# Kernel optimization log

Hardware: AMD Instinct MI355X
Metric: run time of the kernel (lower is better)

Reference implementation:

```python
import jax, jax.numpy as jnp
import numpy as np

PENALTY_LAMBDA = 0.5
MAX_RULES = 512
INIT_GATE_LOGIT = -2.0


def setup_inputs() -> dict:
    key = jax.random.key(0)
    k1, k2, k3 = jax.random.split(key, 3)
    B, V, E = 64, 128000, 1000000
    logits = jax.random.normal(k1, (B, V), dtype=jnp.float32)
    # learned per-rule gate logits (nn.Parameter initialized at init_gate_logit;
    # we perturb slightly so gradients are non-degenerate)
    gate_logits = jnp.full((MAX_RULES,), INIT_GATE_LOGIT, dtype=jnp.float32) \
        + 0.1 * jax.random.normal(k2, (MAX_RULES,), dtype=jnp.float32)
    # flattened ragged (rule, token) violation pairs
    kr, kt = jax.random.split(k3)
    rule_ids = jax.random.randint(kr, (E,), 0, MAX_RULES, dtype=jnp.int32)
    token_ids = jax.random.randint(kt, (E,), 0, V, dtype=jnp.int32)
    return {"logits": logits, "gate_logits": gate_logits,
            "rule_ids": rule_ids, "token_ids": token_ids}


def reference(logits, gate_logits, rule_ids, token_ids):
    # eval-mode binary concrete gate (no noise, no thresholding): sigmoid(logit)
    gates = jax.nn.sigmoid(gate_logits)                      # [R]
    V = logits.shape[-1]
    # gated penalty value per (rule, token) pair, single vectorized scatter-add
    vals = gates[rule_ids] * jnp.asarray(PENALTY_LAMBDA, logits.dtype)  # [E]
    pen_1d = jnp.zeros((V,), dtype=logits.dtype).at[token_ids].add(vals)  # [V]
    penalties = jnp.broadcast_to(pen_1d[None, :], logits.shape)           # [B,V]
    modified = logits - penalties
    # coverage loss: -mean of gates over rules that fire (have >=1 violation)
    firing = jnp.zeros((MAX_RULES,), dtype=logits.dtype).at[rule_ids].set(1.0)
    n_firing = jnp.maximum(firing.sum(), 1.0)
    coverage_loss = -(gates * firing).sum() / n_firing
    return modified, coverage_loss, penalties
```

## Files before the change

### kernel.cpp

```cpp
#include <hip/hip_runtime.h>

#define PENALTY_LAMBDA 0.5f
#define RULES 512
#define NR 4
#define RS 32000
#define VOCAB 128000
#define G 64
#define NQ 2

typedef float f32x4 __attribute__((ext_vector_type(4)));


__global__ void __launch_bounds__(512) scatter_kernel(
    const int* __restrict__ rule_ids, const int* __restrict__ token_ids,
    const float* __restrict__ gate_logits, float* __restrict__ partials,
    unsigned* __restrict__ masks, int E) {
    __shared__ __align__(16) float hist[RS];
    __shared__ float s_g[RULES];
    __shared__ unsigned char s_f[RULES];
    int t = threadIdx.x;
    int g = blockIdx.x;
    int r = blockIdx.y;
    for (int i = t; i < RS; i += 512) hist[i] = 0.f;
    if (t < RULES) {
        float x = gate_logits[t];
        s_g[t] = PENALTY_LAMBDA / (1.0f + expf(-x));
    }
    if (t < RULES / 4) ((unsigned*)s_f)[t] = 0u;
    __syncthreads();

    const int lo = r * RS;
    const int stride = G * 512 * 4;
    for (int base = (g * 512 + t) * 4; base + 4 <= E; base += stride) {
        int4 tt = *(const int4*)(token_ids + base);
        int4 rr = *(const int4*)(rule_ids + base);
        int ts[4] = {tt.x, tt.y, tt.z, tt.w};
        int rv[4] = {rr.x, rr.y, rr.z, rr.w};
#pragma unroll
        for (int k = 0; k < 4; ++k) {
            int tok = ts[k] - lo;
            if ((unsigned)tok < (unsigned)RS) atomicAdd(&hist[tok], s_g[rv[k]]);
            if (r == 0) s_f[rv[k]] = 1;
        }
    }
    if (g == 0 && t == 0) {
        for (int e = E & ~3; e < E; ++e) {
            int tok = token_ids[e] - lo; int ru = rule_ids[e];
            if ((unsigned)tok < (unsigned)RS) atomicAdd(&hist[tok], s_g[ru]);
            if (r == 0) s_f[ru] = 1;
        }
    }
    __syncthreads();

    float* dst = partials + ((size_t)r * G + g) * RS;
    for (int i = t * 4; i < RS; i += 512 * 4)
        *(f32x4*)(dst + i) = *(const f32x4*)(&hist[i]);

    if (r == 0 && t < 16) {
        const unsigned* w = (const unsigned*)s_f + t * 8;
        unsigned m = 0;
#pragma unroll
        for (int k = 0; k < 8; ++k) {
            unsigned d = w[k];
            if (d & 0x000000FFu) m |= 1u << (k * 4 + 0);
            if (d & 0x0000FF00u) m |= 1u << (k * 4 + 1);
            if (d & 0x00FF0000u) m |= 1u << (k * 4 + 2);
            if (d & 0xFF000000u) m |= 1u << (k * 4 + 3);
        }
        masks[g * 16 + t] = m;
    }
}

__global__ void __launch_bounds__(256) reduce_loss_kernel(
    const float* __restrict__ partials, const unsigned* __restrict__ masks,
    const float* __restrict__ gate_logits,
    float* __restrict__ penh, float* __restrict__ out_loss) {
    int t = threadIdx.x;
    int q = blockIdx.y;
    int j = blockIdx.x * 256 + t;
    int v0 = j << 2;
    int r = v0 / RS, bin = v0 - r * RS;
    const float* basep = partials + ((size_t)r * G + (size_t)q * (G / NQ)) * RS + bin;
    f32x4 s = {0.f, 0.f, 0.f, 0.f};
#pragma unroll 4
    for (int g = 0; g < G / NQ; ++g)
        s += *(const f32x4*)(basep + (size_t)g * RS);
    *(f32x4*)(penh + (size_t)q * VOCAB + v0) = s;

    if (blockIdx.x == 0 && q == 0) {
        __shared__ unsigned s_mask[16];
        __shared__ float sg[4], sf[4];
        if (t < 16) {
            unsigned m = 0;
            for (int g = 0; g < G; ++g) m |= masks[g * 16 + t];
            s_mask[t] = m;
        }
        __syncthreads();
        float f = 0.f, gf = 0.f;
        for (int i = t; i < RULES; i += 256) {
            float fb = ((s_mask[i >> 5] >> (i & 31)) & 1u) ? 1.f : 0.f;
            f += fb;
            gf += fb / (1.f + expf(-gate_logits[i]));
        }
        for (int off = 32; off > 0; off >>= 1) {
            gf += __shfl_down(gf, off, 64);
            f  += __shfl_down(f,  off, 64);
        }
        if ((t & 63) == 0) { sg[t >> 6] = gf; sf[t >> 6] = f; }
        __syncthreads();
        if (t == 0) {
            float tg = sg[0] + sg[1] + sg[2] + sg[3];
            float tf = sf[0] + sf[1] + sf[2] + sf[3];
            *out_loss = -tg / fmaxf(tf, 1.0f);
        }
    }
}

__global__ void __launch_bounds__(256) broadcast_kernel(
    const float* __restrict__ logits, const float* __restrict__ penh,
    float* __restrict__ out_mod, float* __restrict__ out_pen) {
    int j = blockIdx.x * 256 + threadIdx.x;
    int b = blockIdx.y;
    int v0 = j << 2;
    size_t base = (size_t)b * VOCAB + v0;
    f32x4 p0 = *(const f32x4*)(penh + v0) + *(const f32x4*)(penh + VOCAB + v0);
    f32x4 l = *(const f32x4*)(logits + base);
    *(f32x4*)(out_mod + base) = l - p0;

    bool lastj = (j == VOCAB / 4 - 1);
    f32x4 p1;
    if (lastj)
        p1 = *(const f32x4*)(penh) + *(const f32x4*)(penh + VOCAB);
    else
        p1 = *(const f32x4*)(penh + v0 + 4) + *(const f32x4*)(penh + VOCAB + v0 + 4);
    f32x4 ps = {p0.w, p1.x, p1.y, p1.z};
    if (lastj && b == (int)gridDim.y - 1) {
        out_pen[base + 3] = p0.w;
    } else {
        *(f32x4*)(out_pen + base + 3) = ps;
    }
    if (j == 0 && b == 0) {
        out_pen[0] = p0.x; out_pen[1] = p0.y; out_pen[2] = p0.z;
    }
}

extern "C" void kernel_launch(void* const* d_in, const int* in_sizes, int n_in,
                              void* d_out, int out_size, void* d_ws, size_t ws_size,
                              hipStream_t stream) {
    const float* logits      = (const float*)d_in[0];
    const float* gate_logits = (const float*)d_in[1];
    const int*   rule_ids    = (const int*)d_in[2];
    const int*   token_ids   = (const int*)d_in[3];
    float* out = (float*)d_out;

    const int E = in_sizes[2];
    const int V = VOCAB;
    const int B = in_sizes[0] / V;
    const size_t BV = (size_t)B * (size_t)V;

    float*    partials = (float*)d_ws;
    float*    penh     = partials + (size_t)NR * G * RS;
    unsigned* masks    = (unsigned*)(penh + (size_t)NQ * VOCAB);

    scatter_kernel<<<dim3(G, NR), 512, 0, stream>>>(
        rule_ids, token_ids, gate_logits, partials, masks, E);

    reduce_loss_kernel<<<dim3(V / 4 / 256, NQ), 256, 0, stream>>>(
        partials, masks, gate_logits, penh, out + BV);

    broadcast_kernel<<<dim3(V / 4 / 256, B), 256, 0, stream>>>(
        logits, penh, out, out + BV + 1);
}
```

Baseline: 130.4 us.

## Fuse partial-histogram reduction, loss, and broadcast into one kernel

New measurement: 122.4 us. 6.1% less time.

```diff
diff --git a/kernel.cpp b/kernel.cpp
--- a/kernel.cpp
+++ b/kernel.cpp
@@ -6,7 +6,9 @@
 #define RS 32000
 #define VOCAB 128000
 #define G 64
-#define NQ 2
+#define NB 64
+#define CH 500
+#define CJ 125
 
 typedef float f32x4 __attribute__((ext_vector_type(4)));
 
@@ -71,37 +73,61 @@
     }
 }
 
-__global__ void __launch_bounds__(256) reduce_loss_kernel(
+__global__ void __launch_bounds__(512) fused_kernel(
     const float* __restrict__ partials, const unsigned* __restrict__ masks,
-    const float* __restrict__ gate_logits,
-    float* __restrict__ penh, float* __restrict__ out_loss) {
+    const float* __restrict__ gate_logits, const float* __restrict__ logits,
+    float* __restrict__ out_mod, float* __restrict__ out_pen,
+    float* __restrict__ out_loss) {
+    __shared__ float s_pc[CH + 4];
+    __shared__ f32x4 s_part[4][CJ + 1];
     int t = threadIdx.x;
-    int q = blockIdx.y;
-    int j = blockIdx.x * 256 + t;
-    int v0 = j << 2;
-    int r = v0 / RS, bin = v0 - r * RS;
-    const float* basep = partials + ((size_t)r * G + (size_t)q * (G / NQ)) * RS + bin;
-    f32x4 s = {0.f, 0.f, 0.f, 0.f};
+    int tx = t & 127, ty = t >> 7;
+    int chunk = blockIdx.x;
+    int c0 = chunk * CH;
+    int r = c0 / RS;
+    int bin = c0 - r * RS;
+
+    {
+        f32x4 acc = {0.f, 0.f, 0.f, 0.f};
+        if (tx < CJ) {
+            const float* bp = partials + (size_t)r * G * RS + bin + tx * 4
+                            + (size_t)(ty * 16) * RS;
 #pragma unroll 4
-    for (int g = 0; g < G / NQ; ++g)
-        s += *(const f32x4*)(basep + (size_t)g * RS);
-    *(f32x4*)(penh + (size_t)q * VOCAB + v0) = s;
+            for (int g = 0; g < 16; ++g)
+                acc += *(const f32x4*)(bp + (size_t)g * RS);
+            s_part[ty][tx] = acc;
+        } else if (tx == 127) {
+            f32x4 e = {0.f, 0.f, 0.f, 0.f};
+            for (int i = 0; i < 4; ++i) {
+                int gb = c0 + CH + i; if (gb >= VOCAB) gb -= VOCAB;
+                int r2 = gb / RS, b2 = gb - r2 * RS;
+                const float* bp2 = partials + (size_t)r2 * G * RS + b2
+                                 + (size_t)(ty * 16) * RS;
+                float s = 0.f;
+                for (int g = 0; g < 16; ++g) s += bp2[(size_t)g * RS];
+                ((float*)&e)[i] = s;
+            }
+            s_part[ty][CJ] = e;
+        }
+    }
+    __syncthreads();
+    if (t < CJ + 1) {
+        f32x4 s = s_part[0][t] + s_part[1][t] + s_part[2][t] + s_part[3][t];
+        *(f32x4*)(s_pc + t * 4) = s;
+    }
+    __syncthreads();
 
-    if (blockIdx.x == 0 && q == 0) {
+    if (chunk == 0) {
         __shared__ unsigned s_mask[16];
-        __shared__ float sg[4], sf[4];
+        __shared__ float sg[8], sf[8];
         if (t < 16) {
             unsigned m = 0;
             for (int g = 0; g < G; ++g) m |= masks[g * 16 + t];
             s_mask[t] = m;
         }
         __syncthreads();
-        float f = 0.f, gf = 0.f;
-        for (int i = t; i < RULES; i += 256) {
-            float fb = ((s_mask[i >> 5] >> (i & 31)) & 1u) ? 1.f : 0.f;
-            f += fb;
-            gf += fb / (1.f + expf(-gate_logits[i]));
-        }
+        float f = ((s_mask[t >> 5] >> (t & 31)) & 1u) ? 1.f : 0.f;
+        float gf = f / (1.f + expf(-gate_logits[t]));
         for (int off = 32; off > 0; off >>= 1) {
             gf += __shfl_down(gf, off, 64);
             f  += __shfl_down(f,  off, 64);
@@ -109,38 +135,32 @@
         if ((t & 63) == 0) { sg[t >> 6] = gf; sf[t >> 6] = f; }
         __syncthreads();
         if (t == 0) {
-            float tg = sg[0] + sg[1] + sg[2] + sg[3];
-            float tf = sf[0] + sf[1] + sf[2] + sf[3];
+            float tg = 0.f, tf = 0.f;
+            for (int w = 0; w < 8; ++w) { tg += sg[w]; tf += sf[w]; }
             *out_loss = -tg / fmaxf(tf, 1.0f);
+            out_pen[0] = s_pc[0];
+            out_pen[1] = s_pc[1];
+            out_pen[2] = s_pc[2];
         }
     }
-}
 
-__global__ void __launch_bounds__(256) broadcast_kernel(
-    const float* __restrict__ logits, const float* __restrict__ penh,
-    float* __restrict__ out_mod, float* __restrict__ out_pen) {
-    int j = blockIdx.x * 256 + threadIdx.x;
-    int b = blockIdx.y;
-    int v0 = j << 2;
-    size_t base = (size_t)b * VOCAB + v0;
-    f32x4 p0 = *(const f32x4*)(penh + v0) + *(const f32x4*)(penh + VOCAB + v0);
-    f32x4 l = *(const f32x4*)(logits + base);
-    *(f32x4*)(out_mod + base) = l - p0;
-
-    bool lastj = (j == VOCAB / 4 - 1);
-    f32x4 p1;
-    if (lastj)
-        p1 = *(const f32x4*)(penh) + *(const f32x4*)(penh + VOCAB);
-    else
-        p1 = *(const f32x4*)(penh + v0 + 4) + *(const f32x4*)(penh + VOCAB + v0 + 4);
-    f32x4 ps = {p0.w, p1.x, p1.y, p1.z};
-    if (lastj && b == (int)gridDim.y - 1) {
-        out_pen[base + 3] = p0.w;
-    } else {
-        *(f32x4*)(out_pen + base + 3) = ps;
-    }
-    if (j == 0 && b == 0) {
-        out_pen[0] = p0.x; out_pen[1] = p0.y; out_pen[2] = p0.z;
+    if (tx >= CJ) return;
+    f32x4 p0 = *(const f32x4*)(s_pc + tx * 4);
+    f32x4 ps = {s_pc[tx * 4 + 3], s_pc[tx * 4 + 4],
+                s_pc[tx * 4 + 5], s_pc[tx * 4 + 6]};
+    bool glast = (chunk == 255 && tx == CJ - 1);
+    size_t col = (size_t)c0 + tx * 4;
+#pragma unroll 4
+    for (int ib = 0; ib < NB / 4; ++ib) {
+        int b = ib * 4 + ty;
+        size_t base = (size_t)b * VOCAB + col;
+        f32x4 l = *(const f32x4*)(logits + base);
+        *(f32x4*)(out_mod + base) = l - p0;
+        if (glast && b == NB - 1) {
+            out_pen[base + 3] = p0.w;
+        } else {
+            *(f32x4*)(out_pen + base + 3) = ps;
+        }
     }
 }
 
@@ -154,20 +174,15 @@
     float* out = (float*)d_out;
 
     const int E = in_sizes[2];
-    const int V = VOCAB;
-    const int B = in_sizes[0] / V;
-    const size_t BV = (size_t)B * (size_t)V;
+    const size_t BV = (size_t)NB * VOCAB;
 
     float*    partials = (float*)d_ws;
-    float*    penh     = partials + (size_t)NR * G * RS;
-    unsigned* masks    = (unsigned*)(penh + (size_t)NQ * VOCAB);
+    unsigned* masks    = (unsigned*)(partials + (size_t)NR * G * RS);
 
     scatter_kernel<<<dim3(G, NR), 512, 0, stream>>>(
         rule_ids, token_ids, gate_logits, partials, masks, E);
 
-    reduce_loss_kernel<<<dim3(V / 4 / 256, NQ), 256, 0, stream>>>(
-        partials, masks, gate_logits, penh, out + BV);
-
-    broadcast_kernel<<<dim3(V / 4 / 256, B), 256, 0, stream>>>(
-        logits, penh, out, out + BV + 1);
+    fused_kernel<<<VOCAB / CH, 512, 0, stream>>>(
+        partials, masks, gate_logits, logits,
+        out, out + BV + 1, out + BV);
 }
```
